# Performance work log

Hardware: AMD Instinct MI355X
Metric: run time of the kernel (lower is better)

The kernel has to match this reference:

```python
import jax, jax.numpy as jnp
import numpy as np

D_MODEL = 1024
N_HEADS = 16
HEAD_DIM = D_MODEL // N_HEADS
EPS = 1e-5


def _rope_tables(T, dim, dtype):
    inv_freq = 1.0 / (10000.0 ** (np.arange(0, dim, 2, dtype=np.float32) / dim))
    t = np.arange(T, dtype=np.float32)
    freqs = np.einsum('i,j->ij', t, inv_freq)            # [T, dim/2]
    emb = np.concatenate([freqs, freqs], axis=-1)        # [T, dim]
    return jnp.asarray(np.cos(emb), dtype), jnp.asarray(np.sin(emb), dtype)


def _rotate(x, cos, sin):
    # x: [B, T, H, hd]; cos/sin: [T, hd] broadcast over B, H
    c = cos[None, :, None, :]
    s = sin[None, :, None, :]
    x1, x2 = jnp.split(x, 2, axis=-1)
    return x * c + jnp.concatenate([-x2, x1], axis=-1) * s


def setup_inputs() -> dict:
    key = jax.random.key(0)
    k1, k2, k3 = jax.random.split(key, 3)
    B, T = 2, 2048
    x = jax.random.normal(k1, (B, T, D_MODEL), jnp.float32)
    norm_w = jnp.ones((D_MODEL,), jnp.float32)
    w_qkv = jax.random.normal(k2, (D_MODEL, 3 * D_MODEL), jnp.float32) * (D_MODEL ** -0.5)
    w_out = jax.random.normal(k3, (D_MODEL, D_MODEL), jnp.float32) * (D_MODEL ** -0.5)
    return {"x": x, "norm_w": norm_w, "w_qkv": w_qkv, "w_out": w_out}


def reference(x, norm_w, w_qkv, w_out):
    B, T, D = x.shape
    residual = x
    # RMSNorm
    h = x * jax.lax.rsqrt(jnp.mean(x * x, axis=-1, keepdims=True) + EPS) * norm_w
    # QKV projection
    qkv = (h @ w_qkv).reshape(B, T, 3, N_HEADS, HEAD_DIM)
    q, k, v = qkv[:, :, 0], qkv[:, :, 1], qkv[:, :, 2]   # [B, T, H, hd]
    # RoPE
    cos, sin = _rope_tables(T, HEAD_DIM, x.dtype)
    q = _rotate(q, cos, sin)
    k = _rotate(k, cos, sin)
    # Non-causal scaled dot-product attention
    scale = HEAD_DIM ** -0.5
    scores = jnp.einsum('bqhd,bkhd->bhqk', q, k) * scale
    attn = jax.nn.softmax(scores, axis=-1)
    out = jnp.einsum('bhqk,bkhd->bqhd', attn, v).reshape(B, T, D)
    return residual + out @ w_out
```

## Files before the change

### kernel.cpp

```cpp
#include <hip/hip_runtime.h>
#include <hip/hip_bf16.h>

typedef float f32x4 __attribute__((ext_vector_type(4)));
typedef __bf16 bf16x8 __attribute__((ext_vector_type(8)));
typedef __bf16 bf16x4 __attribute__((ext_vector_type(4)));

#define D_MODEL 1024
#define T_SEQ   2048
#define NH      16
#define HD      64

__device__ __forceinline__ void gload16(const void* g, void* l) {
    __builtin_amdgcn_global_load_lds(
        (const __attribute__((address_space(1))) unsigned int*)g,
        (__attribute__((address_space(3))) unsigned int*)l, 16, 0, 0);
}

__global__ __launch_bounds__(256) void k_prep(const float* __restrict__ x,
                                              const float* __restrict__ nw,
                                              const float* __restrict__ w_qkv,
                                              const float* __restrict__ w_out,
                                              __bf16* __restrict__ h,
                                              __bf16* __restrict__ wqkvT,
                                              __bf16* __restrict__ woutT,
                                              float2* __restrict__ tab) {
    __shared__ float tile[32][33];
    __shared__ float red[4];
    const int b = blockIdx.x;
    const int tid = threadIdx.x;

    if (b < 4096) {
        const float* src; __bf16* dst; int R, C, bx, by;
        if (b < 3072) { src = w_qkv; dst = wqkvT; R = 1024; C = 3072; bx = b % 96; by = b / 96; }
        else { int b2 = b - 3072; src = w_out; dst = woutT; R = 1024; C = 1024; bx = b2 % 32; by = b2 / 32; }
        int tx = tid & 31, ty = tid >> 5;
        int c0 = bx * 32, r0 = by * 32;
#pragma unroll
        for (int dy = 0; dy < 32; dy += 8)
            tile[ty + dy][tx] = src[(size_t)(r0 + ty + dy) * C + c0 + tx];
        __syncthreads();
#pragma unroll
        for (int dy = 0; dy < 32; dy += 8)
            dst[(size_t)(c0 + ty + dy) * R + r0 + tx] = (__bf16)tile[tx][ty + dy];
    } else if (b < 8192) {
        int row = b - 4096;
        const float4 v = ((const float4*)(x + (size_t)row * D_MODEL))[tid];
        float ss = v.x * v.x + v.y * v.y + v.z * v.z + v.w * v.w;
#pragma unroll
        for (int off = 32; off > 0; off >>= 1) ss += __shfl_down(ss, off, 64);
        if ((tid & 63) == 0) red[tid >> 6] = ss;
        __syncthreads();
        float total = red[0] + red[1] + red[2] + red[3];
        float rms = rsqrtf(total * (1.f / 1024.f) + 1e-5f);
        const float4 wv = ((const float4*)nw)[tid];
        bf16x4 o;
        o[0] = (__bf16)(v.x * rms * wv.x);
        o[1] = (__bf16)(v.y * rms * wv.y);
        o[2] = (__bf16)(v.z * rms * wv.z);
        o[3] = (__bf16)(v.w * rms * wv.w);
        ((bf16x4*)(h + (size_t)row * D_MODEL))[tid] = o;
    } else {
        int idx = (b - 8192) * 256 + tid;
        int t = idx >> 5, i = idx & 31;
        float inv = __builtin_amdgcn_exp2f(-(float)i * 0.41524101186f);
        float ang = (float)t * inv;
        tab[idx] = make_float2(cosf(ang), sinf(ang));
    }
}

template <int EPI, int BM, int BN, int WM, int WN, int THREADS, int LB, int BXC>
__global__ __launch_bounds__(THREADS, LB)
void k_gemm(const __bf16* __restrict__ A,
            const __bf16* __restrict__ Bt, int K,
            const float2* __restrict__ tab,
            __bf16* __restrict__ Qr,
            __bf16* __restrict__ Kr,
            __bf16* __restrict__ Vt,
            const float* __restrict__ resid,
            float* __restrict__ outf) {
    constexpr int MI = BM / WM / 16;
    constexpr int NF = BN / WN / 16;
    constexpr int T8 = THREADS / 8;
    constexpr int NL = BM / T8 + BN / T8;
    __shared__ __bf16 ldsA[2 * BM * 64];
    __shared__ __bf16 ldsB[2 * BN * 64];
    const int tid  = threadIdx.x;
    const int lane = tid & 63;
    const int wave = tid >> 6;
    const int g    = lane >> 4;
    const int lr   = lane & 15;
    const int lin = blockIdx.x;
    const int xcd = lin & 7;
    const int j   = lin >> 3;
    const int bx  = xcd * BXC + j % BXC;
    const int by  = j / BXC;
    const int tile_m = by * BM;
    const int tile_n = bx * BN;
    const int wm = (wave / WN) * (BM / WM);
    const int wn = (wave % WN) * (BN / WN);
    f32x4 acc[MI][NF] = {};

    char* ldsAc = (char*)ldsA;
    char* ldsBc = (char*)ldsB;
    const int srow  = lane >> 3;
    const int sslot = lane & 7;

    auto stage = [&](int buf, int k0) {
#pragma unroll
        for (int i = 0; i < BM / T8; i++) {
            int rbase = i * T8 + wave * 8;
            int row = rbase + srow;
            int sc = (sslot ^ (row & 7)) * 8;
            gload16(A + (size_t)(tile_m + row) * K + k0 + sc,
                    ldsAc + buf * (BM * 128) + rbase * 128);
        }
#pragma unroll
        for (int i = 0; i < BN / T8; i++) {
            int rbase = i * T8 + wave * 8;
            int row = rbase + srow;
            int sc = (sslot ^ (row & 7)) * 8;
            gload16(Bt + (size_t)(tile_n + row) * K + k0 + sc,
                    ldsBc + buf * (BN * 128) + rbase * 128);
        }
    };

    const int NT = K / 64;
    stage(0, 0);
    for (int kt = 0; kt < NT; kt++) {
        const int cur = kt & 1;
        if (kt + 1 < NT) {
            stage(cur ^ 1, (kt + 1) * 64);
            if constexpr (NL == 4)      asm volatile("s_waitcnt vmcnt(4)" ::: "memory");
            else if constexpr (NL == 6) asm volatile("s_waitcnt vmcnt(6)" ::: "memory");
            else                        asm volatile("s_waitcnt vmcnt(0)" ::: "memory");
        } else {
            asm volatile("s_waitcnt vmcnt(0)" ::: "memory");
        }
        __builtin_amdgcn_s_barrier();
        asm volatile("" ::: "memory");

        const char* Ab = ldsAc + cur * (BM * 128);
        const char* Bb = ldsBc + cur * (BN * 128);
#pragma unroll
        for (int kc = 0; kc < 2; kc++) {
            int s = kc * 4 + g;
            bf16x8 af[MI], bfr[NF];
#pragma unroll
            for (int mi = 0; mi < MI; mi++) {
                int row = wm + mi * 16 + lr;
                af[mi] = *(const bf16x8*)(Ab + row * 128 + ((s ^ (row & 7)) << 4));
            }
#pragma unroll
            for (int nf = 0; nf < NF; nf++) {
                int row = wn + nf * 16 + lr;
                bfr[nf] = *(const bf16x8*)(Bb + row * 128 + ((s ^ (row & 7)) << 4));
            }
#pragma unroll
            for (int mi = 0; mi < MI; mi++)
#pragma unroll
                for (int nf = 0; nf < NF; nf++)
                    acc[mi][nf] = __builtin_amdgcn_mfma_f32_16x16x32_bf16(
                        af[mi], bfr[nf], acc[mi][nf], 0, 0, 0);
        }
        asm volatile("s_waitcnt lgkmcnt(0)" ::: "memory");
        __builtin_amdgcn_s_barrier();
        asm volatile("" ::: "memory");
    }

    if constexpr (EPI == 0) {
        const int nb  = tile_n + wn;
        const int sec = nb >> 10;
        const int hh  = (nb & 1023) >> 6;
        if (sec < 2) {
            __bf16* dstbase = (sec == 0) ? Qr : Kr;
            const float sc = (sec == 0) ? 0.180336880111f : 1.0f;
#pragma unroll
            for (int mi = 0; mi < MI; mi++) {
#pragma unroll
                for (int r = 0; r < 4; r++) {
                    int m = tile_m + wm + mi * 16 + g * 4 + r;
                    int bb = m >> 11, t = m & 2047;
                    float2 cs0 = tab[t * 32 + lr];
                    float2 cs1 = tab[t * 32 + 16 + lr];
                    float x0 = acc[mi][0][r], x1 = acc[mi][1][r];
                    float x2 = acc[mi][2][r], x3 = acc[mi][3][r];
                    __bf16* dst = dstbase + ((size_t)(bb * NH + hh) * T_SEQ + t) * HD + lr;
                    dst[0]  = (__bf16)((x0 * cs0.x - x2 * cs0.y) * sc);
                    dst[16] = (__bf16)((x1 * cs1.x - x3 * cs1.y) * sc);
                    dst[32] = (__bf16)((x2 * cs0.x + x0 * cs0.y) * sc);
                    dst[48] = (__bf16)((x3 * cs1.x + x1 * cs1.y) * sc);
                }
            }
        } else {
#pragma unroll
            for (int mi = 0; mi < MI; mi++) {
                int m0 = tile_m + wm + mi * 16 + g * 4;
                int bb = m0 >> 11, t0 = m0 & 2047;
#pragma unroll
                for (int nf = 0; nf < 4; nf++) {
                    int d = nf * 16 + lr;
                    bf16x4 pv;
                    pv[0] = (__bf16)acc[mi][nf][0];
                    pv[1] = (__bf16)acc[mi][nf][1];
                    pv[2] = (__bf16)acc[mi][nf][2];
                    pv[3] = (__bf16)acc[mi][nf][3];
                    *(bf16x4*)(Vt + ((size_t)(bb * NH + hh) * HD + d) * T_SEQ + t0) = pv;
                }
            }
        }
    } else {
#pragma unroll
        for (int mi = 0; mi < MI; mi++)
#pragma unroll
            for (int r = 0; r < 4; r++) {
                int m = tile_m + wm + mi * 16 + g * 4 + r;
#pragma unroll
                for (int nf = 0; nf < NF; nf++) {
                    int n = tile_n + wn + nf * 16 + lr;
                    size_t idx = (size_t)m * D_MODEL + n;
                    outf[idx] = resid[idx] + acc[mi][nf][r];
                }
            }
    }
}

__global__ __launch_bounds__(256, 3) void k_attn(const __bf16* __restrict__ Qr,
                                                 const __bf16* __restrict__ Kr,
                                                 const __bf16* __restrict__ Vt,
                                                 __bf16* __restrict__ aout) {
    __shared__ __bf16 ldsK[2][64 * 64];
    __shared__ __bf16 ldsV[2][64 * 64];
    __shared__ __bf16 plds_all[4][32 * 64];
    const int lane = threadIdx.x & 63;
    const int wave = threadIdx.x >> 6;
    const int g  = lane >> 4;
    const int lr = lane & 15;

    const int lin = blockIdx.x;
    const int xcd = lin & 7;
    const int idx = lin >> 3;
    const int bh  = xcd * 4 + (idx >> 4);
    const int qb  = idx & 15;
    const int q0  = qb * 128 + wave * 32;

    const __bf16* Q  = Qr + (size_t)bh * T_SEQ * HD;
    const __bf16* Kp = Kr + (size_t)bh * T_SEQ * HD;
    const __bf16* Vp = Vt + (size_t)bh * HD * T_SEQ;
    char* plds = (char*)plds_all[wave];
    char* Kbase = (char*)&ldsK[0][0];
    char* Vbase = (char*)&ldsV[0][0];

    int kofs[2][4], pwr[4], prd[2];
#pragma unroll
    for (int kc = 0; kc < 2; kc++)
#pragma unroll
        for (int i = 0; i < 4; i++) {
            int row = i * 16 + lr;
            kofs[kc][i] = row * 128 + ((kc * 64 + g * 16) ^ ((row & 7) << 4));
        }
#pragma unroll
    for (int ki = 0; ki < 4; ki++)
        pwr[ki] = lr * 128 + ((ki * 32 + g * 8) ^ ((lr & 7) << 4));
#pragma unroll
    for (int kc = 0; kc < 2; kc++)
        prd[kc] = lr * 128 + ((kc * 64 + g * 16) ^ ((lr & 7) << 4));

    const int srow8 = lane >> 3;
    const int sslot = lane & 7;
    const int scol = (sslot ^ srow8) * 8;
    const int c0 = wave * 2, c1 = wave * 2 + 1;
    const int r0 = c0 * 8 + srow8, r1 = c1 * 8 + srow8;
    const __bf16* kg0 = Kp + (size_t)r0 * HD + scol;
    const __bf16* kg1 = Kp + (size_t)r1 * HD + scol;
    const __bf16* vg0 = Vp + (size_t)r0 * T_SEQ + scol;
    const __bf16* vg1 = Vp + (size_t)r1 * T_SEQ + scol;
    char* Kl0 = Kbase + c0 * 1024;
    char* Kl1 = Kbase + c1 * 1024;
    char* Vl0 = Vbase + c0 * 1024;
    char* Vl1 = Vbase + c1 * 1024;

    bf16x8 qf[2][2];
#pragma unroll
    for (int qi = 0; qi < 2; qi++)
#pragma unroll
        for (int kc = 0; kc < 2; kc++)
            qf[qi][kc] = *(const bf16x8*)(Q + (size_t)(q0 + qi * 16 + lr) * HD +
                                          kc * 32 + g * 8);

    f32x4 o[2][4] = {};
    float lrun[2] = {0.f, 0.f};

    gload16(kg0, Kl0); gload16(kg1, Kl1);
    gload16(vg0, Vl0); gload16(vg1, Vl1);
    kg0 += 64 * HD; kg1 += 64 * HD; vg0 += 64; vg1 += 64;
    __syncthreads();

    for (int tile = 0; tile < 32; tile++) {
        const int bufoff = (tile & 1) << 13;
        if (tile < 31) {
            const int nb = bufoff ^ 8192;
            gload16(kg0, Kl0 + nb); gload16(kg1, Kl1 + nb);
            gload16(vg0, Vl0 + nb); gload16(vg1, Vl1 + nb);
            kg0 += 64 * HD; kg1 += 64 * HD; vg0 += 64; vg1 += 64;
        }

        f32x4 s[2][4];
        __builtin_amdgcn_s_setprio(1);
#pragma unroll
        for (int kc = 0; kc < 2; kc++) {
            bf16x8 kf[4];
#pragma unroll
            for (int ki = 0; ki < 4; ki++)
                kf[ki] = *(const bf16x8*)(Kbase + bufoff + kofs[kc][ki]);
#pragma unroll
            for (int qi = 0; qi < 2; qi++)
#pragma unroll
                for (int ki = 0; ki < 4; ki++)
                    s[qi][ki] = (kc == 0)
                        ? __builtin_amdgcn_mfma_f32_16x16x32_bf16(
                              kf[ki], qf[qi][0], f32x4{0.f, 0.f, 0.f, 0.f}, 0, 0, 0)
                        : __builtin_amdgcn_mfma_f32_16x16x32_bf16(
                              kf[ki], qf[qi][1], s[qi][ki], 0, 0, 0);
        }
        __builtin_amdgcn_s_setprio(0);

#pragma unroll
        for (int qi = 0; qi < 2; qi++) {
            float ts = 0.f;
#pragma unroll
            for (int ki = 0; ki < 4; ki++) {
                float p0 = __builtin_amdgcn_exp2f(s[qi][ki][0]);
                float p1 = __builtin_amdgcn_exp2f(s[qi][ki][1]);
                float p2 = __builtin_amdgcn_exp2f(s[qi][ki][2]);
                float p3 = __builtin_amdgcn_exp2f(s[qi][ki][3]);
                ts += (p0 + p1) + (p2 + p3);
                bf16x4 pk;
                pk[0] = (__bf16)p0; pk[1] = (__bf16)p1;
                pk[2] = (__bf16)p2; pk[3] = (__bf16)p3;
                *(bf16x4*)(plds + qi * 2048 + pwr[ki]) = pk;
            }
            lrun[qi] += ts;
        }

        __builtin_amdgcn_s_setprio(1);
#pragma unroll
        for (int kc = 0; kc < 2; kc++) {
            bf16x8 vf[4];
#pragma unroll
            for (int nf = 0; nf < 4; nf++)
                vf[nf] = *(const bf16x8*)(Vbase + bufoff + kofs[kc][nf]);
            bf16x8 pf0 = *(const bf16x8*)(plds + prd[kc]);
            bf16x8 pf1 = *(const bf16x8*)(plds + 2048 + prd[kc]);
#pragma unroll
            for (int nf = 0; nf < 4; nf++)
                o[0][nf] = __builtin_amdgcn_mfma_f32_16x16x32_bf16(pf0, vf[nf], o[0][nf], 0, 0, 0);
#pragma unroll
            for (int nf = 0; nf < 4; nf++)
                o[1][nf] = __builtin_amdgcn_mfma_f32_16x16x32_bf16(pf1, vf[nf], o[1][nf], 0, 0, 0);
        }
        __builtin_amdgcn_s_setprio(0);
        __syncthreads();
    }

#pragma unroll
    for (int qi = 0; qi < 2; qi++) {
        lrun[qi] += __shfl_xor(lrun[qi], 16, 64);
        lrun[qi] += __shfl_xor(lrun[qi], 32, 64);
    }

    const int bb = bh >> 4, hh = bh & 15;
#pragma unroll
    for (int qi = 0; qi < 2; qi++) {
        float invT[4];
#pragma unroll
        for (int r = 0; r < 4; r++)
            invT[r] = 1.f / __shfl(lrun[qi], g * 4 + r, 64);
#pragma unroll
        for (int r = 0; r < 4; r++) {
            int t = q0 + qi * 16 + g * 4 + r;
#pragma unroll
            for (int nf = 0; nf < 4; nf++) {
                int d = nf * 16 + lr;
                aout[((size_t)(bb * T_SEQ + t)) * D_MODEL + hh * HD + d] =
                    (__bf16)(o[qi][nf][r] * invT[r]);
            }
        }
    }
}

extern "C" void kernel_launch(void* const* d_in, const int* in_sizes, int n_in,
                              void* d_out, int out_size, void* d_ws, size_t ws_size,
                              hipStream_t stream) {
    const float* x      = (const float*)d_in[0];
    const float* norm_w = (const float*)d_in[1];
    const float* w_qkv  = (const float*)d_in[2];
    const float* w_out  = (const float*)d_in[3];
    float* out = (float*)d_out;
    char* ws = (char*)d_ws;

    __bf16* hbuf  = (__bf16*)(ws);
    __bf16* wqkvT = (__bf16*)(ws + ((size_t)8  << 20));
    __bf16* woutT = (__bf16*)(ws + ((size_t)14 << 20));
    float2* tab   = (float2*)(ws + ((size_t)16 << 20));
    __bf16* Qr    = (__bf16*)(ws + ((size_t)17 << 20));
    __bf16* Kr    = (__bf16*)(ws + ((size_t)25 << 20));
    __bf16* Vt    = (__bf16*)(ws + ((size_t)33 << 20));

    k_prep<<<dim3(8448), dim3(256), 0, stream>>>(x, norm_w, w_qkv, w_out,
                                                 hbuf, wqkvT, woutT, tab);
    k_gemm<0, 128, 128, 4, 2, 512, 4, 3>
        <<<dim3(768), dim3(512), 0, stream>>>(hbuf, wqkvT, 1024, tab,
                                              Qr, Kr, Vt, nullptr, nullptr);
    k_attn<<<dim3(512), dim3(256), 0, stream>>>(Qr, Kr, Vt, hbuf);
    k_gemm<1, 128, 64, 2, 2, 256, 4, 2>
        <<<dim3(512), dim3(256), 0, stream>>>(hbuf, woutT, 1024, nullptr,
                                              nullptr, nullptr, nullptr, x, out);
}
```

Before: 185.9 us.

## Use 256x256 tiles with ping-pong MFMA sub-phases for QKV GEMM

Replaces the templated QKV GEMM with a dedicated kernel using 256x256 block tiles (192 blocks, 8 waves each computing 128x64). The inner loop is split into four quadrant sub-phases with barriers and s_setprio around the MFMA bursts so LDS fragment loads interleave with matrix math across waves. The larger tiles are meant to halve global/LDS traffic per FLOP. The trade-off is fewer blocks than CUs (192 on a 256-CU part), more barriers, and higher register pressure. The output GEMM is only de-templated with the same tile parameters.

```diff
diff --git a/kernel.cpp b/kernel.cpp
--- a/kernel.cpp
+++ b/kernel.cpp
@@ -68,20 +68,204 @@
     }
 }
 
-template <int EPI, int BM, int BN, int WM, int WN, int THREADS, int LB, int BXC>
-__global__ __launch_bounds__(THREADS, LB)
-void k_gemm(const __bf16* __restrict__ A,
-            const __bf16* __restrict__ Bt, int K,
-            const float2* __restrict__ tab,
-            __bf16* __restrict__ Qr,
-            __bf16* __restrict__ Kr,
-            __bf16* __restrict__ Vt,
-            const float* __restrict__ resid,
-            float* __restrict__ outf) {
-    constexpr int MI = BM / WM / 16;
-    constexpr int NF = BN / WN / 16;
-    constexpr int T8 = THREADS / 8;
-    constexpr int NL = BM / T8 + BN / T8;
+__global__ __launch_bounds__(512, 2)
+void k_gemm0(const __bf16* __restrict__ A,
+             const __bf16* __restrict__ Bt,
+             const float2* __restrict__ tab,
+             __bf16* __restrict__ Qr,
+             __bf16* __restrict__ Kr,
+             __bf16* __restrict__ Vt) {
+    constexpr int K = 1024;
+    __shared__ __bf16 ldsA[2 * 256 * 64];
+    __shared__ __bf16 ldsB[2 * 256 * 64];
+    const int tid  = threadIdx.x;
+    const int lane = tid & 63;
+    const int wave = tid >> 6;
+    const int g    = lane >> 4;
+    const int lr   = lane & 15;
+
+    const int lin  = blockIdx.x;
+    const int xcd  = lin & 7;
+    const int j    = lin >> 3;
+    const int idx2 = xcd * 24 + j;
+    const int tile_m = (idx2 & 15) * 256;
+    const int tile_n = (idx2 >> 4) * 256;
+    const int wm = (wave >> 2) * 128;
+    const int wn = (wave & 3) * 64;
+
+    f32x4 acc[8][4] = {};
+
+    char* ldsAc = (char*)ldsA;
+    char* ldsBc = (char*)ldsB;
+    const int srow  = lane >> 3;
+    const int sslot = lane & 7;
+    const int scol  = (sslot ^ srow) * 8;
+    const __bf16* As = A  + (size_t)(tile_m + wave * 8 + srow) * K + scol;
+    const __bf16* Bs = Bt + (size_t)(tile_n + wave * 8 + srow) * K + scol;
+
+    auto stage = [&](int buf, int k0) {
+#pragma unroll
+        for (int i = 0; i < 4; i++)
+            gload16(As + k0 + (size_t)i * 64 * K,
+                    ldsAc + buf * 32768 + i * 8192 + wave * 1024);
+#pragma unroll
+        for (int i = 0; i < 4; i++)
+            gload16(Bs + k0 + (size_t)i * 64 * K,
+                    ldsBc + buf * 32768 + i * 8192 + wave * 1024);
+    };
+
+    stage(0, 0);
+    for (int kt = 0; kt < 16; kt++) {
+        const int cur = kt & 1;
+        if (kt < 15) {
+            stage(cur ^ 1, (kt + 1) * 64);
+            asm volatile("s_waitcnt vmcnt(8)" ::: "memory");
+        } else {
+            asm volatile("s_waitcnt vmcnt(0)" ::: "memory");
+        }
+        __builtin_amdgcn_s_barrier();
+        asm volatile("" ::: "memory");
+
+        const char* Ab = ldsAc + cur * 32768;
+        const char* Bb = ldsBc + cur * 32768;
+        bf16x8 af[4][2], bfr[2][2];
+
+#pragma unroll
+        for (int mi = 0; mi < 4; mi++) {
+            const int row = wm + mi * 16 + lr;
+#pragma unroll
+            for (int kc = 0; kc < 2; kc++)
+                af[mi][kc] = *(const bf16x8*)(Ab + row * 128 + (((kc * 4 + g) ^ (row & 7)) << 4));
+        }
+#pragma unroll
+        for (int nf = 0; nf < 2; nf++) {
+            const int row = wn + nf * 16 + lr;
+#pragma unroll
+            for (int kc = 0; kc < 2; kc++)
+                bfr[nf][kc] = *(const bf16x8*)(Bb + row * 128 + (((kc * 4 + g) ^ (row & 7)) << 4));
+        }
+        __builtin_amdgcn_s_setprio(1);
+#pragma unroll
+        for (int kc = 0; kc < 2; kc++)
+#pragma unroll
+            for (int mi = 0; mi < 4; mi++)
+#pragma unroll
+                for (int nf = 0; nf < 2; nf++)
+                    acc[mi][nf] = __builtin_amdgcn_mfma_f32_16x16x32_bf16(
+                        af[mi][kc], bfr[nf][kc], acc[mi][nf], 0, 0, 0);
+        __builtin_amdgcn_s_setprio(0);
+        __builtin_amdgcn_s_barrier();
+        asm volatile("" ::: "memory");
+
+#pragma unroll
+        for (int nf = 0; nf < 2; nf++) {
+            const int row = wn + (nf + 2) * 16 + lr;
+#pragma unroll
+            for (int kc = 0; kc < 2; kc++)
+                bfr[nf][kc] = *(const bf16x8*)(Bb + row * 128 + (((kc * 4 + g) ^ (row & 7)) << 4));
+        }
+        __builtin_amdgcn_s_setprio(1);
+#pragma unroll
+        for (int kc = 0; kc < 2; kc++)
+#pragma unroll
+            for (int mi = 0; mi < 4; mi++)
+#pragma unroll
+                for (int nf = 0; nf < 2; nf++)
+                    acc[mi][nf + 2] = __builtin_amdgcn_mfma_f32_16x16x32_bf16(
+                        af[mi][kc], bfr[nf][kc], acc[mi][nf + 2], 0, 0, 0);
+        __builtin_amdgcn_s_setprio(0);
+        __builtin_amdgcn_s_barrier();
+        asm volatile("" ::: "memory");
+
+#pragma unroll
+        for (int mi = 0; mi < 4; mi++) {
+            const int row = wm + (mi + 4) * 16 + lr;
+#pragma unroll
+            for (int kc = 0; kc < 2; kc++)
+                af[mi][kc] = *(const bf16x8*)(Ab + row * 128 + (((kc * 4 + g) ^ (row & 7)) << 4));
+        }
+        __builtin_amdgcn_s_setprio(1);
+#pragma unroll
+        for (int kc = 0; kc < 2; kc++)
+#pragma unroll
+            for (int mi = 0; mi < 4; mi++)
+#pragma unroll
+                for (int nf = 0; nf < 2; nf++)
+                    acc[mi + 4][nf + 2] = __builtin_amdgcn_mfma_f32_16x16x32_bf16(
+                        af[mi][kc], bfr[nf][kc], acc[mi + 4][nf + 2], 0, 0, 0);
+        __builtin_amdgcn_s_setprio(0);
+        __builtin_amdgcn_s_barrier();
+        asm volatile("" ::: "memory");
+
+#pragma unroll
+        for (int nf = 0; nf < 2; nf++) {
+            const int row = wn + nf * 16 + lr;
+#pragma unroll
+            for (int kc = 0; kc < 2; kc++)
+                bfr[nf][kc] = *(const bf16x8*)(Bb + row * 128 + (((kc * 4 + g) ^ (row & 7)) << 4));
+        }
+        __builtin_amdgcn_s_setprio(1);
+#pragma unroll
+        for (int kc = 0; kc < 2; kc++)
+#pragma unroll
+            for (int mi = 0; mi < 4; mi++)
+#pragma unroll
+                for (int nf = 0; nf < 2; nf++)
+                    acc[mi + 4][nf] = __builtin_amdgcn_mfma_f32_16x16x32_bf16(
+                        af[mi][kc], bfr[nf][kc], acc[mi + 4][nf], 0, 0, 0);
+        __builtin_amdgcn_s_setprio(0);
+        __builtin_amdgcn_s_barrier();
+        asm volatile("" ::: "memory");
+    }
+
+    const int nb  = tile_n + wn;
+    const int sec = nb >> 10;
+    const int hh  = (nb & 1023) >> 6;
+    if (sec < 2) {
+        __bf16* dstbase = (sec == 0) ? Qr : Kr;
+        const float sc = (sec == 0) ? 0.180336880111f : 1.0f;
+#pragma unroll
+        for (int mi = 0; mi < 8; mi++) {
+#pragma unroll
+            for (int r = 0; r < 4; r++) {
+                int m = tile_m + wm + mi * 16 + g * 4 + r;
+                int bb = m >> 11, t = m & 2047;
+                float2 cs0 = tab[t * 32 + lr];
+                float2 cs1 = tab[t * 32 + 16 + lr];
+                float x0 = acc[mi][0][r], x1 = acc[mi][1][r];
+                float x2 = acc[mi][2][r], x3 = acc[mi][3][r];
+                __bf16* dst = dstbase + ((size_t)(bb * NH + hh) * T_SEQ + t) * HD + lr;
+                dst[0]  = (__bf16)((x0 * cs0.x - x2 * cs0.y) * sc);
+                dst[16] = (__bf16)((x1 * cs1.x - x3 * cs1.y) * sc);
+                dst[32] = (__bf16)((x2 * cs0.x + x0 * cs0.y) * sc);
+                dst[48] = (__bf16)((x3 * cs1.x + x1 * cs1.y) * sc);
+            }
+        }
+    } else {
+#pragma unroll
+        for (int mi = 0; mi < 8; mi++) {
+            int m0 = tile_m + wm + mi * 16 + g * 4;
+            int bb = m0 >> 11, t0 = m0 & 2047;
+#pragma unroll
+            for (int nf = 0; nf < 4; nf++) {
+                int d = nf * 16 + lr;
+                bf16x4 pv;
+                pv[0] = (__bf16)acc[mi][nf][0];
+                pv[1] = (__bf16)acc[mi][nf][1];
+                pv[2] = (__bf16)acc[mi][nf][2];
+                pv[3] = (__bf16)acc[mi][nf][3];
+                *(bf16x4*)(Vt + ((size_t)(bb * NH + hh) * HD + d) * T_SEQ + t0) = pv;
+            }
+        }
+    }
+}
+
+__global__ __launch_bounds__(256, 4)
+void k_gemm1(const __bf16* __restrict__ A,
+             const __bf16* __restrict__ Bt,
+             const float* __restrict__ resid,
+             float* __restrict__ outf) {
+    constexpr int K = 1024, BM = 128, BN = 64;
     __shared__ __bf16 ldsA[2 * BM * 64];
     __shared__ __bf16 ldsB[2 * BN * 64];
     const int tid  = threadIdx.x;
@@ -92,13 +276,13 @@
     const int lin = blockIdx.x;
     const int xcd = lin & 7;
     const int j   = lin >> 3;
-    const int bx  = xcd * BXC + j % BXC;
-    const int by  = j / BXC;
+    const int bx  = xcd * 2 + j % 2;
+    const int by  = j / 2;
     const int tile_m = by * BM;
     const int tile_n = bx * BN;
-    const int wm = (wave / WN) * (BM / WM);
-    const int wn = (wave % WN) * (BN / WN);
-    f32x4 acc[MI][NF] = {};
+    const int wm = (wave >> 1) * 64;
+    const int wn = (wave & 1) * 32;
+    f32x4 acc[4][2] = {};
 
     char* ldsAc = (char*)ldsA;
     char* ldsBc = (char*)ldsB;
@@ -107,16 +291,16 @@
 
     auto stage = [&](int buf, int k0) {
 #pragma unroll
-        for (int i = 0; i < BM / T8; i++) {
-            int rbase = i * T8 + wave * 8;
+        for (int i = 0; i < 4; i++) {
+            int rbase = i * 32 + wave * 8;
             int row = rbase + srow;
             int sc = (sslot ^ (row & 7)) * 8;
             gload16(A + (size_t)(tile_m + row) * K + k0 + sc,
                     ldsAc + buf * (BM * 128) + rbase * 128);
         }
 #pragma unroll
-        for (int i = 0; i < BN / T8; i++) {
-            int rbase = i * T8 + wave * 8;
+        for (int i = 0; i < 2; i++) {
+            int rbase = i * 32 + wave * 8;
             int row = rbase + srow;
             int sc = (sslot ^ (row & 7)) * 8;
             gload16(Bt + (size_t)(tile_n + row) * K + k0 + sc,
@@ -124,15 +308,12 @@
         }
     };
 
-    const int NT = K / 64;
     stage(0, 0);
-    for (int kt = 0; kt < NT; kt++) {
+    for (int kt = 0; kt < 16; kt++) {
         const int cur = kt & 1;
-        if (kt + 1 < NT) {
+        if (kt < 15) {
             stage(cur ^ 1, (kt + 1) * 64);
-            if constexpr (NL == 4)      asm volatile("s_waitcnt vmcnt(4)" ::: "memory");
-            else if constexpr (NL == 6) asm volatile("s_waitcnt vmcnt(6)" ::: "memory");
-            else                        asm volatile("s_waitcnt vmcnt(0)" ::: "memory");
+            asm volatile("s_waitcnt vmcnt(6)" ::: "memory");
         } else {
             asm volatile("s_waitcnt vmcnt(0)" ::: "memory");
         }
@@ -144,21 +325,21 @@
 #pragma unroll
         for (int kc = 0; kc < 2; kc++) {
             int s = kc * 4 + g;
-            bf16x8 af[MI], bfr[NF];
-#pragma unroll
-            for (int mi = 0; mi < MI; mi++) {
+            bf16x8 af[4], bfr[2];
+#pragma unroll
+            for (int mi = 0; mi < 4; mi++) {
                 int row = wm + mi * 16 + lr;
                 af[mi] = *(const bf16x8*)(Ab + row * 128 + ((s ^ (row & 7)) << 4));
             }
 #pragma unroll
-            for (int nf = 0; nf < NF; nf++) {
+            for (int nf = 0; nf < 2; nf++) {
                 int row = wn + nf * 16 + lr;
                 bfr[nf] = *(const bf16x8*)(Bb + row * 128 + ((s ^ (row & 7)) << 4));
             }
 #pragma unroll
-            for (int mi = 0; mi < MI; mi++)
-#pragma unroll
-                for (int nf = 0; nf < NF; nf++)
+            for (int mi = 0; mi < 4; mi++)
+#pragma unroll
+                for (int nf = 0; nf < 2; nf++)
                     acc[mi][nf] = __builtin_amdgcn_mfma_f32_16x16x32_bf16(
                         af[mi], bfr[nf], acc[mi][nf], 0, 0, 0);
         }
@@ -167,61 +348,18 @@
         asm volatile("" ::: "memory");
     }
 
-    if constexpr (EPI == 0) {
-        const int nb  = tile_n + wn;
-        const int sec = nb >> 10;
-        const int hh  = (nb & 1023) >> 6;
-        if (sec < 2) {
-            __bf16* dstbase = (sec == 0) ? Qr : Kr;
-            const float sc = (sec == 0) ? 0.180336880111f : 1.0f;
-#pragma unroll
-            for (int mi = 0; mi < MI; mi++) {
-#pragma unroll
-                for (int r = 0; r < 4; r++) {
-                    int m = tile_m + wm + mi * 16 + g * 4 + r;
-                    int bb = m >> 11, t = m & 2047;
-                    float2 cs0 = tab[t * 32 + lr];
-                    float2 cs1 = tab[t * 32 + 16 + lr];
-                    float x0 = acc[mi][0][r], x1 = acc[mi][1][r];
-                    float x2 = acc[mi][2][r], x3 = acc[mi][3][r];
-                    __bf16* dst = dstbase + ((size_t)(bb * NH + hh) * T_SEQ + t) * HD + lr;
-                    dst[0]  = (__bf16)((x0 * cs0.x - x2 * cs0.y) * sc);
-                    dst[16] = (__bf16)((x1 * cs1.x - x3 * cs1.y) * sc);
-                    dst[32] = (__bf16)((x2 * cs0.x + x0 * cs0.y) * sc);
-                    dst[48] = (__bf16)((x3 * cs1.x + x1 * cs1.y) * sc);
-                }
-            }
-        } else {
-#pragma unroll
-            for (int mi = 0; mi < MI; mi++) {
-                int m0 = tile_m + wm + mi * 16 + g * 4;
-                int bb = m0 >> 11, t0 = m0 & 2047;
-#pragma unroll
-                for (int nf = 0; nf < 4; nf++) {
-                    int d = nf * 16 + lr;
-                    bf16x4 pv;
-                    pv[0] = (__bf16)acc[mi][nf][0];
-                    pv[1] = (__bf16)acc[mi][nf][1];
-                    pv[2] = (__bf16)acc[mi][nf][2];
-                    pv[3] = (__bf16)acc[mi][nf][3];
-                    *(bf16x4*)(Vt + ((size_t)(bb * NH + hh) * HD + d) * T_SEQ + t0) = pv;
-                }
-            }
-        }
-    } else {
-#pragma unroll
-        for (int mi = 0; mi < MI; mi++)
-#pragma unroll
-            for (int r = 0; r < 4; r++) {
-                int m = tile_m + wm + mi * 16 + g * 4 + r;
-#pragma unroll
-                for (int nf = 0; nf < NF; nf++) {
-                    int n = tile_n + wn + nf * 16 + lr;
-                    size_t idx = (size_t)m * D_MODEL + n;
-                    outf[idx] = resid[idx] + acc[mi][nf][r];
-                }
-            }
-    }
+#pragma unroll
+    for (int mi = 0; mi < 4; mi++)
+#pragma unroll
+        for (int r = 0; r < 4; r++) {
+            int m = tile_m + wm + mi * 16 + g * 4 + r;
+#pragma unroll
+            for (int nf = 0; nf < 2; nf++) {
+                int n = tile_n + wn + nf * 16 + lr;
+                size_t idx = (size_t)m * D_MODEL + n;
+                outf[idx] = resid[idx] + acc[mi][nf][r];
+            }
+        }
 }
 
 __global__ __launch_bounds__(256, 3) void k_attn(const __bf16* __restrict__ Qr,
@@ -408,11 +546,7 @@
 
     k_prep<<<dim3(8448), dim3(256), 0, stream>>>(x, norm_w, w_qkv, w_out,
                                                  hbuf, wqkvT, woutT, tab);
-    k_gemm<0, 128, 128, 4, 2, 512, 4, 3>
-        <<<dim3(768), dim3(512), 0, stream>>>(hbuf, wqkvT, 1024, tab,
-                                              Qr, Kr, Vt, nullptr, nullptr);
+    k_gemm0<<<dim3(192), dim3(512), 0, stream>>>(hbuf, wqkvT, tab, Qr, Kr, Vt);
     k_attn<<<dim3(512), dim3(256), 0, stream>>>(Qr, Kr, Vt, hbuf);
-    k_gemm<1, 128, 64, 2, 2, 256, 4, 2>
-        <<<dim3(512), dim3(256), 0, stream>>>(hbuf, woutT, 1024, nullptr,
-                                              nullptr, nullptr, nullptr, x, out);
+    k_gemm1<<<dim3(512), dim3(256), 0, stream>>>(hbuf, woutT, x, out);
 }
```

New measurement: 185.8 us. Within noise of the previous version (-0.1%).
